# Kernel optimization log

Measured on AMD Instinct MI355X. Metric: run time of the kernel, lower is better.

Reference implementation:

```python
import jax, jax.numpy as jnp
import numpy as np

NUM_HEADS = 8


def setup_inputs() -> dict:
    key = jax.random.key(0)
    ks = jax.random.split(key, 5)
    B, C, H, W = 2, 256, 64, 64
    # 0.02 scaling keeps logits in a sane range so softmax is not one-hot
    return {
        "x": jax.random.normal(ks[0], (B, C, H, W), dtype=jnp.float32),
        "w_qkv": jax.random.normal(ks[1], (3 * C, C), dtype=jnp.float32) * 0.02,
        "b_qkv": jax.random.normal(ks[2], (3 * C,), dtype=jnp.float32) * 0.02,
        "w_proj": jax.random.normal(ks[3], (C, C), dtype=jnp.float32) * 0.02,
        "b_proj": jax.random.normal(ks[4], (C,), dtype=jnp.float32) * 0.02,
    }


def reference(x, w_qkv, b_qkv, w_proj, b_proj):
    B, C, H, W = x.shape
    N = H * W
    h = NUM_HEADS
    d = C // h
    # 1x1 conv == per-pixel linear: (B,C,H,W) -> (B,3C,H,W)
    qkv = jnp.einsum('oc,bchw->bohw', w_qkv, x) + b_qkv[None, :, None, None]
    qkv = qkv.reshape(B, 3, h, d, N)
    # q,k,v: (B, h, N, d)
    q = jnp.swapaxes(qkv[:, 0], -2, -1)
    k = jnp.swapaxes(qkv[:, 1], -2, -1)
    v = jnp.swapaxes(qkv[:, 2], -2, -1)
    scale = d ** (-0.5)
    attn = jax.nn.softmax(jnp.einsum('bhnd,bhmd->bhnm', q, k) * scale, axis=-1)
    out = jnp.einsum('bhnm,bhmd->bhnd', attn, v)  # (B, h, N, d)
    # faithful to torch: transpose(1,2) -> (B,N,h,d), then row-major reshape to (B,C,H,W)
    out = jnp.swapaxes(out, 1, 2).reshape(B, C, H, W)
    out = jnp.einsum('oc,bchw->bohw', w_proj, out) + b_proj[None, :, None, None]
    return out
```

## Files before the change

kernel.cpp:

```cpp
#include <hip/hip_runtime.h>
#include <hip/hip_bf16.h>


typedef __bf16 bf16;
typedef __bf16 bf16x4 __attribute__((ext_vector_type(4)));
typedef __bf16 bf16x8 __attribute__((ext_vector_type(8)));
typedef float  f32x4  __attribute__((ext_vector_type(4)));
typedef short  s16x4  __attribute__((ext_vector_type(4)));

#if __has_builtin(__builtin_amdgcn_mfma_f32_16x16x16bf16_1k)
#define HAVE_MFMA16 1
#endif

#if __has_builtin(__builtin_amdgcn_exp2f)
#define EXP2(x) __builtin_amdgcn_exp2f(x)
#else
#define EXP2(x) exp2f(x)
#endif

#define NS 4096
#define QSCALE (0.17677669529663687f * 1.4426950408889634f)

static __device__ inline unsigned pack2(float a, float b) {
  union { bf16 h[2]; unsigned u; } v;
  v.h[0] = (bf16)a; v.h[1] = (bf16)b;
  return v.u;
}

__global__ __launch_bounds__(256) void qkv_fused(
    const float* __restrict__ x, const float* __restrict__ w,
    const float* __restrict__ bias,
    bf16* __restrict__ qbuf, bf16* __restrict__ kbuf, bf16* __restrict__ vbuf)
{
  __shared__ bf16 As[64 * 264];
  __shared__ bf16 Bs[64 * 264];
  const int n0 = blockIdx.x * 64, o0 = blockIdx.y * 64, b = blockIdx.z;
  const int t = threadIdx.x;
  const int wv = t >> 6, L = t & 63, quad = L >> 4, lb = L & 15;

  {
    unsigned* A32 = (unsigned*)As;
    const int nj = (t & 15) * 4;
#pragma unroll
    for (int p = 0; p < 8; p++) {
      const int c = p * 32 + (t >> 4) * 2;
      const float* xr = x + ((size_t)(b * 256 + c)) * NS + n0 + nj;
      f32x4 va = *(const f32x4*)xr;
      f32x4 vb = *(const f32x4*)(xr + NS);
#pragma unroll
      for (int i = 0; i < 4; i++)
        A32[(nj + i) * 132 + (c >> 1)] = pack2(va[i], vb[i]);
    }
  }
  {
    const int cj = (t & 15) * 16;
#pragma unroll
    for (int p = 0; p < 4; p++) {
      const int r = p * 16 + (t >> 4);
      const float* wr = w + (size_t)(o0 + r) * 256 + cj;
      f32x4 w0 = *(const f32x4*)wr,       w1 = *(const f32x4*)(wr + 4);
      f32x4 w2 = *(const f32x4*)(wr + 8), w3 = *(const f32x4*)(wr + 12);
      bf16x8 lo, hi;
#pragma unroll
      for (int i = 0; i < 4; i++) {
        lo[i] = (bf16)w0[i]; lo[4 + i] = (bf16)w1[i];
        hi[i] = (bf16)w2[i]; hi[4 + i] = (bf16)w3[i];
      }
      *(bf16x8*)&Bs[r * 264 + cj] = lo;
      *(bf16x8*)&Bs[r * 264 + cj + 8] = hi;
    }
  }
  __syncthreads();

  f32x4 acc[4] = {};
#pragma unroll
  for (int ks = 0; ks < 8; ks++) {
    const bf16x8 bfr = *(const bf16x8*)&Bs[(wv * 16 + lb) * 264 + ks * 32 + quad * 8];
#pragma unroll
    for (int a = 0; a < 4; a++) {
      const bf16x8 afr = *(const bf16x8*)&As[(a * 16 + lb) * 264 + ks * 32 + quad * 8];
      acc[a] = __builtin_amdgcn_mfma_f32_16x16x32_bf16(afr, bfr, acc[a], 0, 0, 0);
    }
  }

  const int comp = o0 >> 8;
  const int o = o0 + wv * 16 + lb;
  const float bv = bias[o];
  if (comp < 2) {
    bf16* dst = (comp == 0) ? qbuf : kbuf;
    const float sc = (comp == 0) ? QSCALE : 1.0f;
    const int hh = (o & 255) >> 5, dd = o & 31;
    const size_t base = ((size_t)b * 8 + hh) * NS;
#pragma unroll
    for (int a = 0; a < 4; a++)
#pragma unroll
      for (int r = 0; r < 4; r++) {
        const int n = n0 + a * 16 + quad * 4 + r;
        dst[(base + n) * 32 + dd] = (bf16)((acc[a][r] + bv) * sc);
      }
  } else {
    __syncthreads();
    bf16* Vt2 = As;
#pragma unroll
    for (int a = 0; a < 4; a++)
#pragma unroll
      for (int r = 0; r < 4; r++)
        Vt2[(wv * 16 + lb) * 72 + a * 16 + quad * 4 + r] = (bf16)(acc[a][r] + bv);
    __syncthreads();
    const int row = t & 63;
    const int o2 = o0 + row;
    const int hh2 = (o2 & 255) >> 5, dd2 = o2 & 31;
    const int hc = (t >> 6) * 16;
    bf16x8 v0 = *(const bf16x8*)&Vt2[row * 72 + hc];
    bf16x8 v1 = *(const bf16x8*)&Vt2[row * 72 + hc + 8];
    bf16* vd = vbuf + (((size_t)b * 8 + hh2) * 32 + dd2) * NS + n0 + hc;
    *(bf16x8*)vd = v0;
    *(bf16x8*)(vd + 8) = v1;
  }
}

#define KS_OFF 0
#define VT_OFF 2560
#define KV_SZ  (2560 + 32 * 72)

__global__ __launch_bounds__(256) void attn_kernel(
    const bf16* __restrict__ qbuf, const bf16* __restrict__ kbuf,
    const bf16* __restrict__ vbuf, bf16* __restrict__ abuf)
{
  __shared__ bf16 KV[2][KV_SZ];
#ifndef HAVE_MFMA16
  __shared__ bf16 Ps[4][16 * 72];
#endif

  const int qb = blockIdx.x;
  const int bh = blockIdx.y;
  const bf16* Q  = qbuf + (size_t)bh * NS * 32;
  const bf16* K  = kbuf + (size_t)bh * NS * 32;
  const bf16* Vt = vbuf + (size_t)bh * 32 * NS;

  const int t = threadIdx.x;
  const int wv = t >> 6, L = t & 63, quad = L >> 4, lb = L & 15;
  const int qrow = qb * 128 + wv * 32;

  const bf16x8 qfrag0 = *(const bf16x8*)(Q + (size_t)(qrow + lb) * 32 + quad * 8);
  const bf16x8 qfrag1 = *(const bf16x8*)(Q + (size_t)(qrow + 16 + lb) * 32 + quad * 8);

  const int koff = (t >> 2) * 40 + (t & 3) * 8;
  const int voff = VT_OFF + (t >> 3) * 72 + (t & 7) * 8;
  const bf16* gk = K + (size_t)(t >> 2) * 32 + (t & 3) * 8;
  const bf16* gv = Vt + (size_t)(t >> 3) * NS + (t & 7) * 8;

  bf16x8 regk = *(const bf16x8*)gk;
  bf16x8 regv = *(const bf16x8*)gv;

  f32x4 oa0 = {0.f, 0.f, 0.f, 0.f}, oa1 = {0.f, 0.f, 0.f, 0.f};
  f32x4 oa2 = {0.f, 0.f, 0.f, 0.f}, oa3 = {0.f, 0.f, 0.f, 0.f};
  f32x4 oa4 = {0.f, 0.f, 0.f, 0.f}, oa5 = {0.f, 0.f, 0.f, 0.f};
  const f32x4 zero4 = {0.f, 0.f, 0.f, 0.f};
#ifdef HAVE_MFMA16
  const s16x4 ones = {(short)0x3F80, (short)0x3F80, (short)0x3F80, (short)0x3F80};
#else
  float l0_i = 0.f, l1_i = 0.f;
#endif

#pragma unroll 2
  for (int kt = 0; kt < 64; kt++) {
    const int buf = kt & 1;
    *(bf16x8*)&KV[buf][koff] = regk;
    *(bf16x8*)&KV[buf][voff] = regv;
    __syncthreads();
    if (kt < 63) {
      regk = *(const bf16x8*)(gk + (size_t)(kt + 1) * (64 * 32));
      regv = *(const bf16x8*)(gv + (size_t)(kt + 1) * 64);
    }

    f32x4 st0[4], st1[4];
#pragma unroll
    for (int bi = 0; bi < 4; bi++) {
      const bf16x8 kf = *(const bf16x8*)&KV[buf][(bi * 16 + lb) * 40 + quad * 8];
      st0[bi] = __builtin_amdgcn_mfma_f32_16x16x32_bf16(kf, qfrag0, zero4, 0, 0, 0);
      st1[bi] = __builtin_amdgcn_mfma_f32_16x16x32_bf16(kf, qfrag1, zero4, 0, 0, 0);
    }

#pragma unroll
    for (int bi = 0; bi < 4; bi++)
#pragma unroll
      for (int r = 0; r < 4; r++) {
        st0[bi][r] = EXP2(st0[bi][r]);
        st1[bi][r] = EXP2(st1[bi][r]);
      }

#ifdef HAVE_MFMA16
#pragma unroll
    for (int bi = 0; bi < 4; bi++) {
      bf16x4 pb0, pb1;
#pragma unroll
      for (int r = 0; r < 4; r++) {
        pb0[r] = (bf16)st0[bi][r];
        pb1[r] = (bf16)st1[bi][r];
      }
      const s16x4 pf0 = __builtin_bit_cast(s16x4, pb0);
      const s16x4 pf1 = __builtin_bit_cast(s16x4, pb1);
      const s16x4 vf0 = __builtin_bit_cast(s16x4,
          *(const bf16x4*)&KV[buf][VT_OFF + lb * 72 + bi * 16 + quad * 4]);
      const s16x4 vf1 = __builtin_bit_cast(s16x4,
          *(const bf16x4*)&KV[buf][VT_OFF + (16 + lb) * 72 + bi * 16 + quad * 4]);
      oa0 = __builtin_amdgcn_mfma_f32_16x16x16bf16_1k(pf0, vf0, oa0, 0, 0, 0);
      oa1 = __builtin_amdgcn_mfma_f32_16x16x16bf16_1k(pf0, vf1, oa1, 0, 0, 0);
      oa2 = __builtin_amdgcn_mfma_f32_16x16x16bf16_1k(pf0, ones, oa2, 0, 0, 0);
      oa3 = __builtin_amdgcn_mfma_f32_16x16x16bf16_1k(pf1, vf0, oa3, 0, 0, 0);
      oa4 = __builtin_amdgcn_mfma_f32_16x16x16bf16_1k(pf1, vf1, oa4, 0, 0, 0);
      oa5 = __builtin_amdgcn_mfma_f32_16x16x16bf16_1k(pf1, ones, oa5, 0, 0, 0);
    }
#else
    {
      float ls0 = 0.f, ls1 = 0.f;
#pragma unroll
      for (int bi = 0; bi < 4; bi++)
#pragma unroll
        for (int r = 0; r < 4; r++) { ls0 += st0[bi][r]; ls1 += st1[bi][r]; }
      l0_i += ls0; l1_i += ls1;
      bf16* P = &Ps[wv][0];
#pragma unroll
      for (int bi = 0; bi < 4; bi++) {
        bf16x4 pk;
#pragma unroll
        for (int r = 0; r < 4; r++) pk[r] = (bf16)st0[bi][r];
        *(bf16x4*)&P[lb * 72 + bi * 16 + quad * 4] = pk;
      }
#pragma unroll
      for (int ch = 0; ch < 2; ch++) {
        const bf16x8 pf  = *(const bf16x8*)&P[lb * 72 + ch * 32 + quad * 8];
        const bf16x8 vf0 = *(const bf16x8*)&KV[buf][VT_OFF + lb * 72 + ch * 32 + quad * 8];
        const bf16x8 vf1 = *(const bf16x8*)&KV[buf][VT_OFF + (16 + lb) * 72 + ch * 32 + quad * 8];
        oa0 = __builtin_amdgcn_mfma_f32_16x16x32_bf16(pf, vf0, oa0, 0, 0, 0);
        oa1 = __builtin_amdgcn_mfma_f32_16x16x32_bf16(pf, vf1, oa1, 0, 0, 0);
      }
#pragma unroll
      for (int bi = 0; bi < 4; bi++) {
        bf16x4 pk;
#pragma unroll
        for (int r = 0; r < 4; r++) pk[r] = (bf16)st1[bi][r];
        *(bf16x4*)&P[lb * 72 + bi * 16 + quad * 4] = pk;
      }
#pragma unroll
      for (int ch = 0; ch < 2; ch++) {
        const bf16x8 pf  = *(const bf16x8*)&P[lb * 72 + ch * 32 + quad * 8];
        const bf16x8 vf0 = *(const bf16x8*)&KV[buf][VT_OFF + lb * 72 + ch * 32 + quad * 8];
        const bf16x8 vf1 = *(const bf16x8*)&KV[buf][VT_OFF + (16 + lb) * 72 + ch * 32 + quad * 8];
        oa3 = __builtin_amdgcn_mfma_f32_16x16x32_bf16(pf, vf0, oa3, 0, 0, 0);
        oa4 = __builtin_amdgcn_mfma_f32_16x16x32_bf16(pf, vf1, oa4, 0, 0, 0);
      }
    }
#endif
  }

  const int b_ = bh >> 3;
  const int hh = bh & 7;
#ifdef HAVE_MFMA16
#pragma unroll
  for (int r = 0; r < 4; r++) {
#if __has_builtin(__builtin_amdgcn_rcpf)
    const float inv0 = __builtin_amdgcn_rcpf(oa2[r]);
    const float inv1 = __builtin_amdgcn_rcpf(oa5[r]);
#else
    const float inv0 = 1.0f / oa2[r];
    const float inv1 = 1.0f / oa5[r];
#endif
    const int n0_ = qrow + quad * 4 + r;
    const int n1_ = qrow + 16 + quad * 4 + r;
    bf16* dst0 = abuf + ((size_t)b_ * NS + n0_) * 256 + hh * 32;
    bf16* dst1 = abuf + ((size_t)b_ * NS + n1_) * 256 + hh * 32;
    dst0[lb]      = (bf16)(oa0[r] * inv0);
    dst0[16 + lb] = (bf16)(oa1[r] * inv0);
    dst1[lb]      = (bf16)(oa3[r] * inv1);
    dst1[16 + lb] = (bf16)(oa4[r] * inv1);
  }
#else
  float lf0 = l0_i, lf1 = l1_i;
  lf0 += __shfl_xor(lf0, 16); lf0 += __shfl_xor(lf0, 32);
  lf1 += __shfl_xor(lf1, 16); lf1 += __shfl_xor(lf1, 32);
#pragma unroll
  for (int r = 0; r < 4; r++) {
    const float lr0 = __shfl(lf0, (quad << 4) | (quad * 4 + r));
    const float lr1 = __shfl(lf1, (quad << 4) | (quad * 4 + r));
    const float inv0 = 1.0f / lr0;
    const float inv1 = 1.0f / lr1;
    const int n0_ = qrow + quad * 4 + r;
    const int n1_ = qrow + 16 + quad * 4 + r;
    bf16* dst0 = abuf + ((size_t)b_ * NS + n0_) * 256 + hh * 32;
    bf16* dst1 = abuf + ((size_t)b_ * NS + n1_) * 256 + hh * 32;
    dst0[lb]      = (bf16)(oa0[r] * inv0);
    dst0[16 + lb] = (bf16)(oa1[r] * inv0);
    dst1[lb]      = (bf16)(oa3[r] * inv1);
    dst1[16 + lb] = (bf16)(oa4[r] * inv1);
  }
#endif
}

__global__ __launch_bounds__(256) void proj_fused(
    const bf16* __restrict__ abuf, const float* __restrict__ w,
    const float* __restrict__ bias, float* __restrict__ out)
{
  __shared__ bf16 As[64 * 264];
  __shared__ bf16 Bs[64 * 264];
  const int ch0 = blockIdx.x * 64, o0 = blockIdx.y * 64;
  const int z = blockIdx.z, b = z >> 4, sHi = z & 15;
  const int t = threadIdx.x;
  const int wv = t >> 6, L = t & 63, quad = L >> 4, lb = L & 15;

  {
    const int cj = (t & 15) * 16;
#pragma unroll
    for (int p = 0; p < 4; p++) {
      const int r = p * 16 + (t >> 4);
      const float* wr = w + (size_t)(o0 + r) * 256 + cj;
      f32x4 w0 = *(const f32x4*)wr,       w1 = *(const f32x4*)(wr + 4);
      f32x4 w2 = *(const f32x4*)(wr + 8), w3 = *(const f32x4*)(wr + 12);
      bf16x8 lo, hi;
#pragma unroll
      for (int i = 0; i < 4; i++) {
        lo[i] = (bf16)w0[i]; lo[4 + i] = (bf16)w1[i];
        hi[i] = (bf16)w2[i]; hi[4 + i] = (bf16)w3[i];
      }
      *(bf16x8*)&As[r * 264 + cj] = lo;
      *(bf16x8*)&As[r * 264 + cj + 8] = hi;
    }
  }
  {
    const int chj = (t & 7) * 8;
#pragma unroll
    for (int p = 0; p < 8; p++) {
      const int c = p * 32 + (t >> 3);
      bf16x8 v = *(const bf16x8*)(abuf +
          ((size_t)b * NS + (size_t)c * 16 + sHi) * 256 + ch0 + chj);
#pragma unroll
      for (int i = 0; i < 8; i++) Bs[(chj + i) * 264 + c] = v[i];
    }
  }
  __syncthreads();

  f32x4 acc[4] = {};
#pragma unroll
  for (int ks = 0; ks < 8; ks++) {
    const bf16x8 bfr = *(const bf16x8*)&Bs[(wv * 16 + lb) * 264 + ks * 32 + quad * 8];
#pragma unroll
    for (int a = 0; a < 4; a++) {
      const bf16x8 afr = *(const bf16x8*)&As[(a * 16 + lb) * 264 + ks * 32 + quad * 8];
      acc[a] = __builtin_amdgcn_mfma_f32_16x16x32_bf16(afr, bfr, acc[a], 0, 0, 0);
    }
  }

  const int ch = ch0 + wv * 16 + lb;
#pragma unroll
  for (int a = 0; a < 4; a++)
#pragma unroll
    for (int r = 0; r < 4; r++) {
      const int o = o0 + a * 16 + quad * 4 + r;
      out[((size_t)b * 256 + o) * NS + sHi * 256 + ch] = acc[a][r] + bias[o];
    }
}

extern "C" void kernel_launch(void* const* d_in, const int* in_sizes, int n_in,
                              void* d_out, int out_size, void* d_ws, size_t ws_size,
                              hipStream_t stream) {
  const float* x      = (const float*)d_in[0];
  const float* w_qkv  = (const float*)d_in[1];
  const float* b_qkv  = (const float*)d_in[2];
  const float* w_proj = (const float*)d_in[3];
  const float* b_proj = (const float*)d_in[4];
  float* out = (float*)d_out;

  char* ws = (char*)d_ws;
  const size_t MB = 1024 * 1024;
  bf16* qbuf = (bf16*)(ws);
  bf16* kbuf = (bf16*)(ws + 4 * MB);
  bf16* vbuf = (bf16*)(ws + 8 * MB);
  bf16* abuf = (bf16*)(ws + 12 * MB);

  qkv_fused<<<dim3(64, 12, 2), 256, 0, stream>>>(x, w_qkv, b_qkv, qbuf, kbuf, vbuf);
  attn_kernel<<<dim3(32, 16), 256, 0, stream>>>(qbuf, kbuf, vbuf, abuf);
  proj_fused<<<dim3(4, 4, 32), 256, 0, stream>>>(abuf, w_proj, b_proj, out);
}
```

Measured before the change: 158.5 us.

## Split attention over two KV halves and merge partials in projection kernel

The attention kernel now processes half of the keys per block along a new grid dimension, doubling the number of blocks. It writes unnormalized fp32 partial outputs and row sums instead of the normalized bf16 output. The projection kernel adds the two partials, divides by the combined sum and converts to bf16 while staging its operand. This raises occupancy and parallelism for the attention stage, at the cost of extra global memory traffic for the fp32 partial buffers.

```diff
diff --git a/kernel.cpp b/kernel.cpp
--- a/kernel.cpp
+++ b/kernel.cpp
@@ -119,13 +119,13 @@
   }
 }
 
-#define KS_OFF 0
 #define VT_OFF 2560
 #define KV_SZ  (2560 + 32 * 72)
 
 __global__ __launch_bounds__(256) void attn_kernel(
     const bf16* __restrict__ qbuf, const bf16* __restrict__ kbuf,
-    const bf16* __restrict__ vbuf, bf16* __restrict__ abuf)
+    const bf16* __restrict__ vbuf, float* __restrict__ pbuf,
+    float* __restrict__ lbuf)
 {
   __shared__ bf16 KV[2][KV_SZ];
 #ifndef HAVE_MFMA16
@@ -134,9 +134,11 @@
 
   const int qb = blockIdx.x;
   const int bh = blockIdx.y;
+  const int half = blockIdx.z;
+  const int kv0 = half * 2048;
   const bf16* Q  = qbuf + (size_t)bh * NS * 32;
-  const bf16* K  = kbuf + (size_t)bh * NS * 32;
-  const bf16* Vt = vbuf + (size_t)bh * 32 * NS;
+  const bf16* K  = kbuf + (size_t)bh * NS * 32 + (size_t)kv0 * 32;
+  const bf16* Vt = vbuf + (size_t)bh * 32 * NS + kv0;
 
   const int t = threadIdx.x;
   const int wv = t >> 6, L = t & 63, quad = L >> 4, lb = L & 15;
@@ -164,12 +166,12 @@
 #endif
 
 #pragma unroll 2
-  for (int kt = 0; kt < 64; kt++) {
+  for (int kt = 0; kt < 32; kt++) {
     const int buf = kt & 1;
     *(bf16x8*)&KV[buf][koff] = regk;
     *(bf16x8*)&KV[buf][voff] = regv;
     __syncthreads();
-    if (kt < 63) {
+    if (kt < 31) {
       regk = *(const bf16x8*)(gk + (size_t)(kt + 1) * (64 * 32));
       regv = *(const bf16x8*)(gv + (size_t)(kt + 1) * 64);
     }
@@ -257,50 +259,43 @@
 
   const int b_ = bh >> 3;
   const int hh = bh & 7;
-#ifdef HAVE_MFMA16
-#pragma unroll
-  for (int r = 0; r < 4; r++) {
-#if __has_builtin(__builtin_amdgcn_rcpf)
-    const float inv0 = __builtin_amdgcn_rcpf(oa2[r]);
-    const float inv1 = __builtin_amdgcn_rcpf(oa5[r]);
-#else
-    const float inv0 = 1.0f / oa2[r];
-    const float inv1 = 1.0f / oa5[r];
-#endif
-    const int n0_ = qrow + quad * 4 + r;
-    const int n1_ = qrow + 16 + quad * 4 + r;
-    bf16* dst0 = abuf + ((size_t)b_ * NS + n0_) * 256 + hh * 32;
-    bf16* dst1 = abuf + ((size_t)b_ * NS + n1_) * 256 + hh * 32;
-    dst0[lb]      = (bf16)(oa0[r] * inv0);
-    dst0[16 + lb] = (bf16)(oa1[r] * inv0);
-    dst1[lb]      = (bf16)(oa3[r] * inv1);
-    dst1[16 + lb] = (bf16)(oa4[r] * inv1);
-  }
-#else
+  float* pb = pbuf + ((size_t)(half * 2 + b_) * NS) * 256;
+  float* lsum = lbuf + ((size_t)(half * 2 + b_) * NS) * 8;
+#ifndef HAVE_MFMA16
   float lf0 = l0_i, lf1 = l1_i;
   lf0 += __shfl_xor(lf0, 16); lf0 += __shfl_xor(lf0, 32);
   lf1 += __shfl_xor(lf1, 16); lf1 += __shfl_xor(lf1, 32);
+#endif
 #pragma unroll
   for (int r = 0; r < 4; r++) {
+    const int n0_ = qrow + quad * 4 + r;
+    const int n1_ = n0_ + 16;
+    float* d0 = pb + (size_t)n0_ * 256 + hh * 32;
+    float* d1 = pb + (size_t)n1_ * 256 + hh * 32;
+    d0[lb]      = oa0[r];
+    d0[16 + lb] = oa1[r];
+    d1[lb]      = oa3[r];
+    d1[16 + lb] = oa4[r];
+#ifdef HAVE_MFMA16
+    if (lb == 0) {
+      lsum[(size_t)n0_ * 8 + hh] = oa2[r];
+      lsum[(size_t)n1_ * 8 + hh] = oa5[r];
+    }
+#else
     const float lr0 = __shfl(lf0, (quad << 4) | (quad * 4 + r));
     const float lr1 = __shfl(lf1, (quad << 4) | (quad * 4 + r));
-    const float inv0 = 1.0f / lr0;
-    const float inv1 = 1.0f / lr1;
-    const int n0_ = qrow + quad * 4 + r;
-    const int n1_ = qrow + 16 + quad * 4 + r;
-    bf16* dst0 = abuf + ((size_t)b_ * NS + n0_) * 256 + hh * 32;
-    bf16* dst1 = abuf + ((size_t)b_ * NS + n1_) * 256 + hh * 32;
-    dst0[lb]      = (bf16)(oa0[r] * inv0);
-    dst0[16 + lb] = (bf16)(oa1[r] * inv0);
-    dst1[lb]      = (bf16)(oa3[r] * inv1);
-    dst1[16 + lb] = (bf16)(oa4[r] * inv1);
-  }
-#endif
+    if (lb == 0) {
+      lsum[(size_t)n0_ * 8 + hh] = lr0;
+      lsum[(size_t)n1_ * 8 + hh] = lr1;
+    }
+#endif
+  }
 }
 
 __global__ __launch_bounds__(256) void proj_fused(
-    const bf16* __restrict__ abuf, const float* __restrict__ w,
-    const float* __restrict__ bias, float* __restrict__ out)
+    const float* __restrict__ pbuf, const float* __restrict__ lbuf,
+    const float* __restrict__ w, const float* __restrict__ bias,
+    float* __restrict__ out)
 {
   __shared__ bf16 As[64 * 264];
   __shared__ bf16 Bs[64 * 264];
@@ -329,13 +324,25 @@
   }
   {
     const int chj = (t & 7) * 8;
+    const int hh = (ch0 + chj) >> 5;
 #pragma unroll
     for (int p = 0; p < 8; p++) {
       const int c = p * 32 + (t >> 3);
-      bf16x8 v = *(const bf16x8*)(abuf +
-          ((size_t)b * NS + (size_t)c * 16 + sHi) * 256 + ch0 + chj);
-#pragma unroll
-      for (int i = 0; i < 8; i++) Bs[(chj + i) * 264 + c] = v[i];
+      const int n = c * 16 + sHi;
+      const size_t row0 = (size_t)(0 * 2 + b) * NS + n;
+      const size_t row1 = (size_t)(1 * 2 + b) * NS + n;
+      const float* p0 = pbuf + row0 * 256 + ch0 + chj;
+      const float* p1 = pbuf + row1 * 256 + ch0 + chj;
+      f32x4 a0 = *(const f32x4*)p0,       a1 = *(const f32x4*)(p0 + 4);
+      f32x4 c0 = *(const f32x4*)p1,       c1 = *(const f32x4*)(p1 + 4);
+      const float l0 = lbuf[row0 * 8 + hh];
+      const float l1 = lbuf[row1 * 8 + hh];
+      const float inv = 1.0f / (l0 + l1);
+#pragma unroll
+      for (int i = 0; i < 4; i++) {
+        Bs[(chj + i) * 264 + c]     = (bf16)((a0[i] + c0[i]) * inv);
+        Bs[(chj + 4 + i) * 264 + c] = (bf16)((a1[i] + c1[i]) * inv);
+      }
     }
   }
   __syncthreads();
@@ -373,12 +380,13 @@
 
   char* ws = (char*)d_ws;
   const size_t MB = 1024 * 1024;
-  bf16* qbuf = (bf16*)(ws);
-  bf16* kbuf = (bf16*)(ws + 4 * MB);
-  bf16* vbuf = (bf16*)(ws + 8 * MB);
-  bf16* abuf = (bf16*)(ws + 12 * MB);
+  bf16* qbuf  = (bf16*)(ws);
+  bf16* kbuf  = (bf16*)(ws + 4 * MB);
+  bf16* vbuf  = (bf16*)(ws + 8 * MB);
+  float* pbuf = (float*)(ws + 12 * MB);
+  float* lbuf = (float*)(ws + 28 * MB);
 
   qkv_fused<<<dim3(64, 12, 2), 256, 0, stream>>>(x, w_qkv, b_qkv, qbuf, kbuf, vbuf);
-  attn_kernel<<<dim3(32, 16), 256, 0, stream>>>(qbuf, kbuf, vbuf, abuf);
-  proj_fused<<<dim3(4, 4, 32), 256, 0, stream>>>(abuf, w_proj, b_proj, out);
-}
+  attn_kernel<<<dim3(32, 16, 2), 256, 0, stream>>>(qbuf, kbuf, vbuf, pbuf, lbuf);
+  proj_fused<<<dim3(4, 4, 32), 256, 0, stream>>>(pbuf, lbuf, w_proj, b_proj, out);
+}
```

Result: faster. 150.8 us (-4.8%).
